# Kernel tuning notes

Measured on AMD Instinct MI355X. Metric: run time of the kernel, lower is better.

## Reference

```python
import jax, jax.numpy as jnp
import numpy as np

N = 20000
F_IN = 500
HID = 64
CLS = 16
H = 4
K_KNN = 10
NEG_SLOPE = 0.2


def _edges(key, n_rand):
    # random edges plus self-loops (mirrors add_self_loops in the torch code)
    src = jax.random.randint(key, (n_rand,), 0, N)
    dst = jax.random.randint(jax.random.fold_in(key, 1), (n_rand,), 0, N)
    loops = jnp.arange(N)
    return jnp.stack([jnp.concatenate([src, loops]), jnp.concatenate([dst, loops])]).astype(jnp.int32)


def setup_inputs():
    key = jax.random.key(0)
    ks = jax.random.split(key, 40)
    inp = {}
    inp['x'] = jax.random.normal(ks[0], (N, F_IN), jnp.float32)
    inp['edge_index_1'] = _edges(ks[1], 16 * N)          # 1-hop graph, 340k edges
    inp['edge_index_2'] = _edges(ks[2], 32 * N)          # denser 2-hop graph, 660k edges
    knn_src = jnp.repeat(jnp.arange(N), K_KNN)
    knn_dst = jax.random.randint(ks[3], (K_KNN * N,), 0, N)
    inp['edge_index_knn'] = jnp.stack([knn_src, knn_dst]).astype(jnp.int32)

    def p(k, shape):
        return jax.random.normal(k, shape, jnp.float32) * 0.05

    dims = {1: (F_IN, HID), 2: (HID, CLS), 3: (F_IN, HID), 4: (HID, CLS), 5: (F_IN, HID), 6: (HID, CLS)}
    i = 4
    for j in range(1, 7):
        fi, fo = dims[j]
        inp[f'W{j}'] = p(ks[i], (fi, H, fo)); i += 1
        inp[f'as{j}'] = p(ks[i], (H, fo)); i += 1
        inp[f'ad{j}'] = p(ks[i], (H, fo)); i += 1
        inp[f'b{j}'] = jnp.zeros((fo,), jnp.float32)
    for j in range(1, 4):
        inp[f'lin{j}_w'] = p(ks[i], (CLS, CLS)); i += 1
        inp[f'lin{j}_b'] = jnp.zeros((CLS,), jnp.float32)
    inp['agg_w'] = p(ks[i], (CLS,))
    return inp


def gat_conv(x, ei, W, a_s, a_d, b):
    # PyG GATConv, concat=False (mean over heads). W: [F,H,D], a_s/a_d: [H,D], b: [D]
    src, dst = ei[0], ei[1]
    z = jnp.einsum('nf,fhd->nhd', x, W)                 # [N,H,D]
    e_src = jnp.sum(z * a_s, -1)                         # [N,H]
    e_dst = jnp.sum(z * a_d, -1)                         # [N,H]
    e = jax.nn.leaky_relu(e_src[src] + e_dst[dst], NEG_SLOPE)   # [E,H]
    m = jax.ops.segment_max(e, dst, num_segments=N)      # per-dst softmax (edge softmax)
    p = jnp.exp(e - m[dst])
    s = jax.ops.segment_sum(p, dst, num_segments=N)
    alpha = p / (s[dst] + 1e-16)                         # [E,H]
    out = jax.ops.segment_sum(alpha[:, :, None] * z[src], dst, num_segments=N)  # [N,H,D]
    return out.mean(1) + b


def reference(x, edge_index_1, edge_index_2, edge_index_knn,
              W1, as1, ad1, b1, W2, as2, ad2, b2,
              W3, as3, ad3, b3, W4, as4, ad4, b4,
              W5, as5, ad5, b5, W6, as6, ad6, b6,
              lin1_w, lin1_b, lin2_w, lin2_b, lin3_w, lin3_b, agg_w):
    # eval mode: dropout is a no-op
    h1 = jax.nn.relu(gat_conv(x, edge_index_1, W1, as1, ad1, b1))
    h1 = gat_conv(h1, edge_index_1, W2, as2, ad2, b2)
    h2 = jax.nn.relu(gat_conv(x, edge_index_2, W3, as3, ad3, b3))
    h2 = gat_conv(h2, edge_index_2, W4, as4, ad4, b4)
    h3 = jax.nn.relu(gat_conv(x, edge_index_knn, W5, as5, ad5, b5))
    h3 = gat_conv(h3, edge_index_knn, W6, as6, ad6, b6)

    a1 = jnp.tanh(h1 @ lin1_w + lin1_b) @ agg_w          # [N]
    a2 = jnp.tanh(h2 @ lin2_w + lin2_b) @ agg_w
    a3 = jnp.tanh(h3 @ lin3_w + lin3_b) @ agg_w
    a = jax.nn.softmax(jnp.stack([a1, a2, a3], axis=1), axis=1)  # [N,3]
    h = a[:, 0:1] * h1 + a[:, 1:2] * h2 + a[:, 2:3] * h3
    return jax.nn.log_softmax(h, axis=1)
```

## Files before the change

kernel.cpp:

```cpp
#include <hip/hip_runtime.h>
#include <hip/hip_bf16.h>
#include <math.h>

#define N_NODES 20000
#define MP      20096
#define FIN     500
#define KP      512
#define NBUCK   157

typedef unsigned short u16;
typedef unsigned char  u8;
typedef __attribute__((ext_vector_type(8))) short   short8;
typedef __attribute__((ext_vector_type(2))) unsigned uv2;
typedef __attribute__((ext_vector_type(2))) float   f32x2;
typedef __attribute__((ext_vector_type(4))) float   f32x4;

__device__ __forceinline__ float b2f(u16 u){
  union { unsigned int i; float f; } v; v.i = ((unsigned int)u) << 16; return v.f;
}
__device__ __forceinline__ u16 f2b(float f){
  __hip_bfloat16 h = __float2bfloat16(f);
  return *reinterpret_cast<u16*>(&h);
}
__device__ __forceinline__ float lrelu(float x){ return x >= 0.f ? x : 0.2f * x; }
__device__ __forceinline__ float ldp(const void* p, int i, int bf){
  return bf ? b2f(((const u16*)p)[i]) : ((const float*)p)[i];
}
__device__ __forceinline__ u8 f2fp8(float f){
  return (u8)(__builtin_amdgcn_cvt_pk_fp8_f32(f, 0.f, 0, false) & 0xff);
}
template<bool HI>
__device__ __forceinline__ f32x2 fp8pair(unsigned w){
  return __builtin_amdgcn_cvt_pk_f32_fp8((int)w, HI);
}
__device__ __forceinline__ void gll16(const u16* g, u16* l){
  __builtin_amdgcn_global_load_lds(
      (const __attribute__((address_space(1))) unsigned int*)g,
      (__attribute__((address_space(3))) unsigned int*)l, 16, 0, 0);
}

__global__ void detect_dtype_kernel(const unsigned int* __restrict__ xw, int nwords,
                                    int* __restrict__ flag){
  __shared__ int cnt;
  if (threadIdx.x == 0) cnt = 0;
  __syncthreads();
  int c = 0;
  for (int i = threadIdx.x; i < nwords; i += 256){
    unsigned e = (xw[i] >> 7) & 0xFF;
    if (e >= 0x70 && e <= 0x8F) c++;
  }
  atomicAdd(&cnt, c);
  __syncthreads();
  if (threadIdx.x == 0) *flag = (cnt * 2 > nwords) ? 1 : 0;
}

#define CHA 8192
__global__ __launch_bounds__(256) void prep_kernel(
    const void* __restrict__ x, u16* __restrict__ xp,
    const void* Wb0, const void* Wb1, const void* Wb2,
    const void* Ws0, const void* Ws1, const void* Ws2,
    u16* ob0, u16* ob1, u16* ob2, u16* os0, u16* os1, u16* os2,
    const int* s0, const int* s1, const int* s2,
    const int* d0, const int* d1, const int* d2,
    int E0, int E1, int E2, int S0, int S1, int S2, int EB,
    int* __restrict__ bucketCur, unsigned* p0, unsigned* p1, unsigned* p2,
    const int* __restrict__ flag){
  __shared__ int hb[NBUCK];
  __shared__ int hbase[NBUCK];
  int bf = *flag;
  if (blockIdx.y == 0){
    int t = blockIdx.x * 256 + threadIdx.x;
    if (t >= MP * 64) return;
    int row = t >> 6;
    int j0  = (t & 63) * 8;
    short8 v;
#pragma unroll
    for (int j = 0; j < 8; ++j){
      int k = j0 + j;
      u16 val = 0;
      if (row < N_NODES && k < FIN)
        val = bf ? ((const u16*)x)[(size_t)row * FIN + k]
                 : f2b(((const float*)x)[(size_t)row * FIN + k]);
      v[j] = (short)val;
    }
    *(short8*)(xp + (size_t)row * KP + j0) = v;
  } else if (blockIdx.y == 1){
    int xb = blockIdx.x;
    if (xb >= 6 * 512) return;
    int which = xb >> 9;
    int t = (xb & 511) * 256 + threadIdx.x;
    if (which < 3){
      if (t >= 256 * KP) return;
      const void* W = which == 0 ? Wb0 : (which == 1 ? Wb1 : Wb2);
      u16* O = which == 0 ? ob0 : (which == 1 ? ob1 : ob2);
      int n = t / KP, k = t % KP;
      u16 val = 0;
      if (k < FIN)
        val = bf ? ((const u16*)W)[(size_t)k * 256 + n]
                 : f2b(((const float*)W)[(size_t)k * 256 + n]);
      O[t] = val;
    } else {
      if (t >= 64 * 64) return;
      const void* W = which == 3 ? Ws0 : (which == 4 ? Ws1 : Ws2);
      u16* O = which == 3 ? os0 : (which == 4 ? os1 : os2);
      int n = t / 64, k = t % 64;
      O[t] = bf ? ((const u16*)W)[(size_t)k * 64 + n]
                : f2b(((const float*)W)[(size_t)k * 64 + n]);
    }
  } else {
    int sblk = blockIdx.x;
    if (sblk >= 3 * EB) return;
    int g = sblk / EB;
    const int* src = g == 0 ? s0 : (g == 1 ? s1 : s2);
    const int* dst = g == 0 ? d0 : (g == 1 ? d1 : d2);
    unsigned* pairs = g == 0 ? p0 : (g == 1 ? p1 : p2);
    int E = g == 0 ? E0 : (g == 1 ? E1 : E2);
    int S = g == 0 ? S0 : (g == 1 ? S1 : S2);
    int base = (sblk % EB) * CHA;
    if (base >= E) return;
    for (int i = threadIdx.x; i < NBUCK; i += 256) hb[i] = 0;
    __syncthreads();
    int rk[CHA / 256];
#pragma unroll
    for (int i = 0; i < CHA / 256; ++i){
      int e = base + i * 256 + threadIdx.x;
      rk[i] = 0;
      if (e < E) rk[i] = atomicAdd(&hb[dst[e] >> 7], 1);
    }
    __syncthreads();
    for (int i = threadIdx.x; i < NBUCK; i += 256)
      hbase[i] = atomicAdd(&bucketCur[g * NBUCK + i], hb[i]);
    __syncthreads();
#pragma unroll
    for (int i = 0; i < CHA / 256; ++i){
      int e = base + i * 256 + threadIdx.x;
      if (e < E){
        int d = dst[e];
        int b = d >> 7;
        int pos = hbase[b] + rk[i];
        if (pos < S)
          pairs[(size_t)b * S + pos] = ((unsigned)src[e] << 7) | (unsigned)(d & 127);
      }
    }
  }
}

__global__ __launch_bounds__(256) void csr_finalize_kernel(
    const unsigned* p0, const unsigned* p1, const unsigned* p2,
    int S0, int S1, int S2,
    const int* __restrict__ bucketCur,
    int* e0, int* e1, int* e2,
    int2* __restrict__ metaB){
  int g = blockIdx.y;
  const unsigned* pairs = g == 0 ? p0 : (g == 1 ? p1 : p2);
  int* esrc = g == 0 ? e0 : (g == 1 ? e1 : e2);
  int S = g == 0 ? S0 : (g == 1 ? S1 : S2);
  int2* meta = metaB + (size_t)g * MP;
  int b = blockIdx.x;
  int nb = bucketCur[g * NBUCK + b];
  if (nb > S) nb = S;
  const unsigned* pb = pairs + (size_t)b * S;
  int* eb = esrc + (size_t)b * S;
  __shared__ int cnt[128];
  __shared__ int loff[128];
  __shared__ int cur[128];
  if (threadIdx.x < 128) cnt[threadIdx.x] = 0;
  __syncthreads();
  for (int i = threadIdx.x; i < nb; i += 256)
    atomicAdd(&cnt[pb[i] & 127], 1);
  __syncthreads();
  if (threadIdx.x == 0){
    int run = 0;
    for (int k = 0; k < 128; ++k){ loff[k] = run; run += cnt[k]; }
  }
  __syncthreads();
  if (threadIdx.x < 128){
    cur[threadIdx.x] = loff[threadIdx.x];
    int d = b * 128 + threadIdx.x;
    if (d < N_NODES){
      int2 m; m.x = b * S + loff[threadIdx.x]; m.y = cnt[threadIdx.x];
      meta[d] = m;
    }
  }
  __syncthreads();
  for (int i = threadIdx.x; i < nb; i += 256){
    unsigned u = pb[i];
    int slot = atomicAdd(&cur[u & 127], 1);
    eb[slot] = (int)(u >> 7);
  }
}

__global__ __launch_bounds__(256) void gemm_big_kernel(const u16* __restrict__ A,
    const u16* B0, const u16* B1, const u16* B2,
    u8* C0, u8* C1, u8* C2,
    const void* as0, const void* as1, const void* as2,
    const void* ad0, const void* ad1, const void* ad2,
    float* __restrict__ esB, float* __restrict__ edB,
    const int* __restrict__ flag, int M){
  int g = blockIdx.z;
  const u16* BT = g == 0 ? B0 : (g == 1 ? B1 : B2);
  u8* C = g == 0 ? C0 : (g == 1 ? C1 : C2);
  const void* as_ = g == 0 ? as0 : (g == 1 ? as1 : as2);
  const void* ad_ = g == 0 ? ad0 : (g == 1 ? ad1 : ad2);
  float* es = esB + (size_t)g * N_NODES * 4;
  float* ed = edB + (size_t)g * N_NODES * 4;
  __shared__ alignas(16) u16 As[128 * 64];
  __shared__ alignas(16) u16 Bs[128 * 64];
  const int K = KP, Nn = 256;
  int t = threadIdx.x, lane = t & 63, w = t >> 6;
  int m0 = blockIdx.y * 128, n0 = blockIdx.x * 128;
  int mw = (w >> 1) * 64, nw = (w & 1) * 64;
  f32x4 acc[4][4] = {};
  for (int k0 = 0; k0 < K; k0 += 64){
    __syncthreads();
#pragma unroll
    for (int i = 0; i < 4; ++i){
      int c = i * 256 + w * 64 + lane;
      int row = c >> 3, slot = c & 7;
      int kk = ((slot ^ (row & 7))) * 8;
      gll16(A  + (size_t)(m0 + row) * K + k0 + kk, As + (size_t)(i * 256 + w * 64) * 8);
      gll16(BT + (size_t)(n0 + row) * K + k0 + kk, Bs + (size_t)(i * 256 + w * 64) * 8);
    }
    __syncthreads();
#pragma unroll
    for (int ks = 0; ks < 2; ++ks){
      short8 af[4], bfr[4];
#pragma unroll
      for (int mi = 0; mi < 4; ++mi){
        int row = mw + mi * 16 + (lane & 15);
        int sl = (ks * 4 + (lane >> 4)) ^ (row & 7);
        af[mi] = *(const short8*)(As + (size_t)row * 64 + sl * 8);
      }
#pragma unroll
      for (int ni = 0; ni < 4; ++ni){
        int row = nw + ni * 16 + (lane & 15);
        int sl = (ks * 4 + (lane >> 4)) ^ (row & 7);
        bfr[ni] = *(const short8*)(Bs + (size_t)row * 64 + sl * 8);
      }
#pragma unroll
      for (int mi = 0; mi < 4; ++mi)
#pragma unroll
        for (int ni = 0; ni < 4; ++ni)
          acc[mi][ni] = __builtin_amdgcn_mfma_f32_16x16x32_bf16(af[mi], bfr[ni], acc[mi][ni], 0, 0, 0);
    }
  }
  int bf = *flag;
#pragma unroll
  for (int mi = 0; mi < 4; ++mi)
#pragma unroll
    for (int ni = 0; ni < 4; ++ni)
#pragma unroll
      for (int r = 0; r < 4; ++r){
        int row = m0 + mw + mi * 16 + (lane >> 4) * 4 + r;
        int col = n0 + nw + ni * 16 + (lane & 15);
        if (row < M) C[(size_t)row * Nn + col] = f2fp8(acc[mi][ni][r]);
      }
  {
    int h = (n0 + nw) >> 6;
    float asv[4], adv[4];
#pragma unroll
    for (int ni = 0; ni < 4; ++ni){
      int col = n0 + nw + ni * 16 + (lane & 15);
      asv[ni] = ldp(as_, col, bf);
      adv[ni] = ldp(ad_, col, bf);
    }
#pragma unroll
    for (int mi = 0; mi < 4; ++mi)
#pragma unroll
      for (int r = 0; r < 4; ++r){
        float ps = 0.f, pd2 = 0.f;
#pragma unroll
        for (int ni = 0; ni < 4; ++ni){
          ps  += acc[mi][ni][r] * asv[ni];
          pd2 += acc[mi][ni][r] * adv[ni];
        }
#pragma unroll
        for (int m2 = 1; m2 < 16; m2 <<= 1){
          ps  += __shfl_xor(ps, m2);
          pd2 += __shfl_xor(pd2, m2);
        }
        int row = m0 + mw + mi * 16 + (lane >> 4) * 4 + r;
        if ((lane & 15) == 0 && row < M){
          es[(size_t)row * 4 + h] = ps;
          ed[(size_t)row * 4 + h] = pd2;
        }
      }
  }
}

__global__ __launch_bounds__(256) void gemm_small_kernel(
    const u16* A0, const u16* A1, const u16* A2,
    const u16* B0, const u16* B1, const u16* B2,
    u8* C0, u8* C1, u8* C2,
    const void* as0, const void* as1, const void* as2,
    const void* ad0, const void* ad1, const void* ad2,
    float* __restrict__ esB, float* __restrict__ edB,
    const int* __restrict__ flag, int M){
  int g = blockIdx.y;
  const u16* A  = g == 0 ? A0 : (g == 1 ? A1 : A2);
  const u16* BT = g == 0 ? B0 : (g == 1 ? B1 : B2);
  u8* C = g == 0 ? C0 : (g == 1 ? C1 : C2);
  const void* as_ = g == 0 ? as0 : (g == 1 ? as1 : as2);
  const void* ad_ = g == 0 ? ad0 : (g == 1 ? ad1 : ad2);
  float* es = esB + (size_t)g * N_NODES * 4;
  float* ed = edB + (size_t)g * N_NODES * 4;
  __shared__ alignas(16) u16 As[64 * 64];
  __shared__ alignas(16) u16 Bs[64 * 64];
  int t = threadIdx.x, lane = t & 63, w = t >> 6;
  int m0 = blockIdx.x * 64;
#pragma unroll
  for (int i = 0; i < 2; ++i){
    int c = i * 256 + w * 64 + lane;
    int row = c >> 3, slot = c & 7;
    int kk = ((slot ^ (row & 7))) * 8;
    gll16(A  + (size_t)(m0 + row) * 64 + kk, As + (size_t)(i * 256 + w * 64) * 8);
    gll16(BT + (size_t)row * 64 + kk,        Bs + (size_t)(i * 256 + w * 64) * 8);
  }
  __syncthreads();
  f32x4 acc[4] = {};
  int mw = w * 16;
#pragma unroll
  for (int ks = 0; ks < 2; ++ks){
    int rowa = mw + (lane & 15);
    int sla = (ks * 4 + (lane >> 4)) ^ (rowa & 7);
    short8 af = *(const short8*)(As + (size_t)rowa * 64 + sla * 8);
#pragma unroll
    for (int ni = 0; ni < 4; ++ni){
      int rowb = ni * 16 + (lane & 15);
      int slb = (ks * 4 + (lane >> 4)) ^ (rowb & 7);
      short8 bv = *(const short8*)(Bs + (size_t)rowb * 64 + slb * 8);
      acc[ni] = __builtin_amdgcn_mfma_f32_16x16x32_bf16(af, bv, acc[ni], 0, 0, 0);
    }
  }
  int bf = *flag;
#pragma unroll
  for (int ni = 0; ni < 4; ++ni)
#pragma unroll
    for (int r = 0; r < 4; ++r){
      int row = m0 + mw + (lane >> 4) * 4 + r;
      int col = ni * 16 + (lane & 15);
      if (row < M) C[(size_t)row * 64 + col] = f2fp8(acc[ni][r]);
    }
  {
    float asv[4], adv[4];
#pragma unroll
    for (int ni = 0; ni < 4; ++ni){
      int col = ni * 16 + (lane & 15);
      asv[ni] = ldp(as_, col, bf);
      adv[ni] = ldp(ad_, col, bf);
    }
#pragma unroll
    for (int r = 0; r < 4; ++r){
      float ps[4], pd2[4];
#pragma unroll
      for (int ni = 0; ni < 4; ++ni){ ps[ni] = acc[ni][r] * asv[ni]; pd2[ni] = acc[ni][r] * adv[ni]; }
#pragma unroll
      for (int m2 = 1; m2 < 16; m2 <<= 1)
#pragma unroll
        for (int ni = 0; ni < 4; ++ni){
          ps[ni]  += __shfl_xor(ps[ni], m2);
          pd2[ni] += __shfl_xor(pd2[ni], m2);
        }
      int row = m0 + mw + (lane >> 4) * 4 + r;
      if ((lane & 15) == 0 && row < M){
#pragma unroll
        for (int ni = 0; ni < 4; ++ni){
          es[(size_t)row * 4 + ni] = ps[ni];
          ed[(size_t)row * 4 + ni] = pd2[ni];
        }
      }
    }
  }
}

template<int DT, bool RELU, bool BF16OUT, int PIPE>
__global__ __launch_bounds__(256) void gat_agg5_kernel(
    const u8* z0, const u8* z1, const u8* z2,
    const float* __restrict__ esB, const float* __restrict__ edB,
    const int2* __restrict__ metaB,
    const int* e0p, const int* e1p, const int* e2p,
    const void* b0, const void* b1, const void* b2,
    void* o0, void* o1, void* o2,
    const int* __restrict__ flag){
  int g = blockIdx.y;
  const u8* z = g == 0 ? z0 : (g == 1 ? z1 : z2);
  const int* esrc = g == 0 ? e0p : (g == 1 ? e1p : e2p);
  const void* bias = g == 0 ? b0 : (g == 1 ? b1 : b2);
  void* out = g == 0 ? o0 : (g == 1 ? o1 : o2);
  const float* es = esB + (size_t)g * N_NODES * 4;
  const float* ed = edB + (size_t)g * N_NODES * 4;
  const int2* meta = metaB + (size_t)g * MP;
  int bf = *flag;

  int d = (blockIdx.x * 256 + threadIdx.x) >> 6;
  int lane = threadIdx.x & 63;
  if (d >= N_NODES) return;
  constexpr int LPG = DT / 8;
  constexpr int G   = 64 / LPG;
  constexpr int HD  = DT / 4;
  int grp = lane / LPG;
  int li  = lane % LPG;
  int c0  = li * 8;
  int h   = c0 / HD;

  int2 md = meta[d];
  int deg = md.y;
  const int* ep = esrc + md.x;
  float edh = ed[(unsigned)d * 4 + h];

  float acc[8] = {0,0,0,0,0,0,0,0};
  float sacc = 0.f;

  int steps = (deg + PIPE * G - 1) / (PIPE * G);
  for (int tb = 0; tb < steps; ++tb){
    int e0 = tb * PIPE * G + grp;
    int s[PIPE]; float q[PIPE]; uv2 v[PIPE]; bool val[PIPE];
#pragma unroll
    for (int i = 0; i < PIPE; ++i){
      int e = e0 + i * G;
      val[i] = e < deg;
      int sl = ep[e];
      s[i] = val[i] ? sl : 0;
    }
#pragma unroll
    for (int i = 0; i < PIPE; ++i) q[i] = es[(unsigned)s[i] * 4 + h];
#pragma unroll
    for (int i = 0; i < PIPE; ++i) v[i] = *(const uv2*)(z + (unsigned)s[i] * DT + c0);
#pragma unroll
    for (int i = 0; i < PIPE; ++i){
      float p = val[i] ? __expf(lrelu(q[i] + edh)) : 0.f;
      sacc += p;
      f32x2 a0 = fp8pair<false>(v[i][0]), a1 = fp8pair<true>(v[i][0]);
      f32x2 a2 = fp8pair<false>(v[i][1]), a3 = fp8pair<true>(v[i][1]);
      acc[0] = fmaf(p, a0.x, acc[0]); acc[1] = fmaf(p, a0.y, acc[1]);
      acc[2] = fmaf(p, a1.x, acc[2]); acc[3] = fmaf(p, a1.y, acc[3]);
      acc[4] = fmaf(p, a2.x, acc[4]); acc[5] = fmaf(p, a2.y, acc[5]);
      acc[6] = fmaf(p, a3.x, acc[6]); acc[7] = fmaf(p, a3.y, acc[7]);
    }
  }

#pragma unroll
  for (int m = LPG; m < 64; m <<= 1){
    sacc += __shfl_xor(sacc, m);
#pragma unroll
    for (int j = 0; j < 8; ++j) acc[j] += __shfl_xor(acc[j], m);
  }
  float inv = 1.f / (sacc + 1e-16f);
  float v8[8];
#pragma unroll
  for (int j = 0; j < 8; ++j) v8[j] = acc[j] * inv;
#pragma unroll
  for (int m = HD / 8; m < LPG; m <<= 1)
#pragma unroll
    for (int j = 0; j < 8; ++j) v8[j] += __shfl_xor(v8[j], m);

  if (lane < HD / 8){
    if constexpr (BF16OUT){
      short8 ov;
#pragma unroll
      for (int j = 0; j < 8; ++j){
        float o = v8[j] * 0.25f + ldp(bias, lane * 8 + j, bf);
        if (RELU) o = fmaxf(o, 0.f);
        ov[j] = (short)f2b(o);
      }
      *(short8*)((u16*)out + (size_t)d * HD + lane * 8) = ov;
    } else {
      float o[8];
#pragma unroll
      for (int j = 0; j < 8; ++j){
        o[j] = v8[j] * 0.25f + ldp(bias, lane * 8 + j, bf);
        if (RELU) o[j] = fmaxf(o[j], 0.f);
      }
      float* op = (float*)out + (size_t)d * HD + lane * 8;
      *(float4*)op = make_float4(o[0], o[1], o[2], o[3]);
      *(float4*)(op + 4) = make_float4(o[4], o[5], o[6], o[7]);
    }
  }
}

__global__ __launch_bounds__(256) void final_combine_kernel(
    const float* __restrict__ h1, const float* __restrict__ h2, const float* __restrict__ h3,
    const void* l1w, const void* l1b, const void* l2w, const void* l2b,
    const void* l3w, const void* l3b, const void* aggw,
    void* __restrict__ outv, int n, const int* __restrict__ flag){
  __shared__ float Lw[3][16][16];
  __shared__ float Lb[3][16];
  __shared__ float Ag[16];
  int t = threadIdx.x;
  int bf = *flag;
  {
    const void* ws[3] = { l1w, l2w, l3w };
    for (int g = 0; g < 3; ++g) Lw[g][t / 16][t % 16] = ldp(ws[g], t, bf);
    if (t < 16){
      Lb[0][t] = ldp(l1b, t, bf); Lb[1][t] = ldp(l2b, t, bf); Lb[2][t] = ldp(l3b, t, bf);
      Ag[t] = ldp(aggw, t, bf);
    }
  }
  __syncthreads();
  int node = blockIdx.x * 256 + t;
  if (node >= n) return;
  const float* hp[3] = { h1, h2, h3 };
  float hv[3][16];
  float a[3];
  for (int g = 0; g < 3; ++g){
    const float4* h4 = (const float4*)(hp[g] + (size_t)node * 16);
#pragma unroll
    for (int q = 0; q < 4; ++q){
      float4 f = h4[q];
      hv[g][q * 4 + 0] = f.x; hv[g][q * 4 + 1] = f.y;
      hv[g][q * 4 + 2] = f.z; hv[g][q * 4 + 3] = f.w;
    }
    float dot = 0.f;
#pragma unroll
    for (int j = 0; j < 16; ++j){
      float acc2 = Lb[g][j];
#pragma unroll
      for (int i = 0; i < 16; ++i) acc2 += hv[g][i] * Lw[g][i][j];
      dot += tanhf(acc2) * Ag[j];
    }
    a[g] = dot;
  }
  float am = fmaxf(a[0], fmaxf(a[1], a[2]));
  float e0 = __expf(a[0] - am), e1 = __expf(a[1] - am), e2 = __expf(a[2] - am);
  float einv = 1.f / (e0 + e1 + e2);
  float w0 = e0 * einv, w1 = e1 * einv, w2 = e2 * einv;
  float hh[16];
  float hmax = -INFINITY;
#pragma unroll
  for (int i = 0; i < 16; ++i){
    hh[i] = w0 * hv[0][i] + w1 * hv[1][i] + w2 * hv[2][i];
    hmax = fmaxf(hmax, hh[i]);
  }
  float se = 0.f;
#pragma unroll
  for (int i = 0; i < 16; ++i) se += __expf(hh[i] - hmax);
  float ls = hmax + logf(se);
#pragma unroll
  for (int i = 0; i < 16; ++i){
    float o = hh[i] - ls;
    if (bf) ((__hip_bfloat16*)outv)[(size_t)node * 16 + i] = __float2bfloat16(o);
    else    ((float*)outv)[(size_t)node * 16 + i] = o;
  }
}

extern "C" void kernel_launch(void* const* d_in, const int* in_sizes, int n_in,
                              void* d_out, int out_size, void* d_ws, size_t ws_size,
                              hipStream_t stream){
  const void* x = d_in[0];
  const int* ei[3] = { (const int*)d_in[1], (const int*)d_in[2], (const int*)d_in[3] };
  int E[3] = { in_sizes[1] / 2, in_sizes[2] / 2, in_sizes[3] / 2 };
  int Emax = E[0] > E[1] ? E[0] : E[1]; if (E[2] > Emax) Emax = E[2];
  int EB = (Emax + CHA - 1) / CHA;
  int S[3];
  for (int g = 0; g < 3; ++g){
    long s = ((long)E[g] * 27 / 20) / NBUCK + 64;
    s &= ~63L; if (s > 8192) s = 8192;
    S[g] = (int)s;
  }
  const void *W[6], *as_[6], *ad_[6], *bb[6];
  for (int j = 0; j < 6; ++j){
    W[j]   = d_in[4 + 4 * j];
    as_[j] = d_in[5 + 4 * j];
    ad_[j] = d_in[6 + 4 * j];
    bb[j]  = d_in[7 + 4 * j];
  }
  const void* l1w = d_in[28]; const void* l1b = d_in[29];
  const void* l2w = d_in[30]; const void* l2b = d_in[31];
  const void* l3w = d_in[32]; const void* l3b = d_in[33];
  const void* agg = d_in[34];

  char* p = (char*)d_ws;
  auto alloc = [&](size_t bytes) -> void* {
    void* r = (void*)p;
    p += (bytes + 255) & ~(size_t)255;
    return r;
  };
  int* dflag = (int*)alloc(256);
  u16* xp = (u16*)alloc((size_t)MP * KP * 2);
  u16* hmid[3]; for (int g = 0; g < 3; ++g) hmid[g] = xp + (size_t)g * MP * 64;
  u16* wtb[3]; for (int g = 0; g < 3; ++g) wtb[g] = (u16*)alloc((size_t)256 * KP * 2);
  u16* wts[3]; for (int g = 0; g < 3; ++g) wts[g] = (u16*)alloc((size_t)64 * 64 * 2);
  u8* zf[3];   for (int g = 0; g < 3; ++g) zf[g]  = (u8*)alloc((size_t)N_NODES * 256 + 256);
  float* hbr[3]; for (int g = 0; g < 3; ++g) hbr[g] = (float*)alloc((size_t)N_NODES * 16 * 4);
  float* esB = (float*)alloc((size_t)3 * N_NODES * 4 * 4);
  float* edB = (float*)alloc((size_t)3 * N_NODES * 4 * 4);
  int* bucketCur = (int*)alloc((size_t)3 * NBUCK * 4);
  int2* metaB    = (int2*)alloc((size_t)3 * MP * 8);
  int* esrc[3];
  for (int g = 0; g < 3; ++g) esrc[g] = (int*)alloc(((size_t)NBUCK * S[g] + 256) * 4);
  unsigned* pairs[3];
  for (int g = 0; g < 3; ++g) pairs[g] = (unsigned*)alloc(((size_t)NBUCK * S[g] + 256) * 4);

  const int* s0 = ei[0];          const int* s1 = ei[1];          const int* s2 = ei[2];
  const int* d0 = ei[0] + E[0];   const int* d1 = ei[1] + E[1];   const int* d2 = ei[2] + E[2];

  (void)hipMemsetAsync(bucketCur, 0, (size_t)3 * NBUCK * 4, stream);
  detect_dtype_kernel<<<1, 256, 0, stream>>>((const unsigned int*)x, 16384, dflag);
  prep_kernel<<<dim3((MP * 64 + 255) / 256, 3), 256, 0, stream>>>(
      x, xp, W[0], W[2], W[4], W[1], W[3], W[5],
      wtb[0], wtb[1], wtb[2], wts[0], wts[1], wts[2],
      s0, s1, s2, d0, d1, d2, E[0], E[1], E[2], S[0], S[1], S[2], EB,
      bucketCur, pairs[0], pairs[1], pairs[2], dflag);
  csr_finalize_kernel<<<dim3(NBUCK, 3), 256, 0, stream>>>(
      pairs[0], pairs[1], pairs[2], S[0], S[1], S[2], bucketCur,
      esrc[0], esrc[1], esrc[2], metaB);

  const int convGrid = (N_NODES + 3) / 4;

  gemm_big_kernel<<<dim3(2, MP / 128, 3), 256, 0, stream>>>(
      xp, wtb[0], wtb[1], wtb[2], zf[0], zf[1], zf[2],
      as_[0], as_[2], as_[4], ad_[0], ad_[2], ad_[4], esB, edB, dflag, N_NODES);
  gat_agg5_kernel<256, true, true, 6><<<dim3(convGrid, 3), 256, 0, stream>>>(
      zf[0], zf[1], zf[2], esB, edB, metaB, esrc[0], esrc[1], esrc[2],
      bb[0], bb[2], bb[4], (void*)hmid[0], (void*)hmid[1], (void*)hmid[2], dflag);

  gemm_small_kernel<<<dim3(MP / 64, 3), 256, 0, stream>>>(
      hmid[0], hmid[1], hmid[2], wts[0], wts[1], wts[2], zf[0], zf[1], zf[2],
      as_[1], as_[3], as_[5], ad_[1], ad_[3], ad_[5], esB, edB, dflag, N_NODES);
  gat_agg5_kernel<64, false, false, 4><<<dim3(convGrid, 3), 256, 0, stream>>>(
      zf[0], zf[1], zf[2], esB, edB, metaB, esrc[0], esrc[1], esrc[2],
      bb[1], bb[3], bb[5], (void*)hbr[0], (void*)hbr[1], (void*)hbr[2], dflag);

  final_combine_kernel<<<(N_NODES + 255) / 256, 256, 0, stream>>>(
      hbr[0], hbr[1], hbr[2], l1w, l1b, l2w, l2b, l3w, l3b, agg,
      d_out, N_NODES, dflag);
}
```

Before: 366.5 us.

## Rework prep kernel: vectorized x cast, tiled weight transpose, LDS-staged edge bucketing

Prep and CSR kernels move to 1024-thread blocks. The x conversion now uses vectorized float4/ushort4 loads. Weight transposes go through a 64x65 LDS tile so both reads and writes are coalesced. Edge bucketing sorts each chunk locally in LDS before scattering, so global writes to the pairs buffer are contiguous per bucket. The dtype detection also samples fewer words. In exchange the prep kernel uses much more LDS, and every branch of it pays that allocation.

```diff
diff --git a/kernel.cpp b/kernel.cpp
--- a/kernel.cpp
+++ b/kernel.cpp
@@ -38,14 +38,19 @@
       (const __attribute__((address_space(1))) unsigned int*)g,
       (__attribute__((address_space(3))) unsigned int*)l, 16, 0, 0);
 }
-
-__global__ void detect_dtype_kernel(const unsigned int* __restrict__ xw, int nwords,
-                                    int* __restrict__ flag){
+__device__ __forceinline__ void barrier_lgkm(){
+  asm volatile("s_waitcnt lgkmcnt(0)" ::: "memory");
+  __builtin_amdgcn_s_barrier();
+  asm volatile("" ::: "memory");
+}
+
+__global__ __launch_bounds__(1024) void detect_dtype_kernel(const unsigned int* __restrict__ xw, int nwords,
+                                                            int* __restrict__ flag){
   __shared__ int cnt;
   if (threadIdx.x == 0) cnt = 0;
   __syncthreads();
   int c = 0;
-  for (int i = threadIdx.x; i < nwords; i += 256){
+  for (int i = threadIdx.x; i < nwords; i += 1024){
     unsigned e = (xw[i] >> 7) & 0xFF;
     if (e >= 0x70 && e <= 0x8F) c++;
   }
@@ -55,7 +60,8 @@
 }
 
 #define CHA 8192
-__global__ __launch_bounds__(256) void prep_kernel(
+#define PB  1024
+__global__ __launch_bounds__(PB) void prep_kernel(
     const void* __restrict__ x, u16* __restrict__ xp,
     const void* Wb0, const void* Wb1, const void* Wb2,
     const void* Ws0, const void* Ws1, const void* Ws2,
@@ -66,46 +72,78 @@
     int* __restrict__ bucketCur, unsigned* p0, unsigned* p1, unsigned* p2,
     const int* __restrict__ flag){
   __shared__ int hb[NBUCK];
+  __shared__ int loff[NBUCK];
   __shared__ int hbase[NBUCK];
+  __shared__ unsigned shp[CHA];
+  __shared__ u8 shb[CHA];
+  __shared__ u16 tile[64][65];
   int bf = *flag;
+  int tid = threadIdx.x;
   if (blockIdx.y == 0){
-    int t = blockIdx.x * 256 + threadIdx.x;
+    int t = blockIdx.x * PB + tid;
     if (t >= MP * 64) return;
     int row = t >> 6;
     int j0  = (t & 63) * 8;
-    short8 v;
-#pragma unroll
-    for (int j = 0; j < 8; ++j){
-      int k = j0 + j;
-      u16 val = 0;
-      if (row < N_NODES && k < FIN)
-        val = bf ? ((const u16*)x)[(size_t)row * FIN + k]
-                 : f2b(((const float*)x)[(size_t)row * FIN + k]);
-      v[j] = (short)val;
+    short8 v = {0,0,0,0,0,0,0,0};
+    if (row < N_NODES){
+      if (j0 + 8 <= FIN){
+        if (bf){
+          const ushort4* xr = (const ushort4*)((const u16*)x + (size_t)row * FIN + j0);
+          ushort4 a = xr[0], b = xr[1];
+          v[0]=(short)a.x; v[1]=(short)a.y; v[2]=(short)a.z; v[3]=(short)a.w;
+          v[4]=(short)b.x; v[5]=(short)b.y; v[6]=(short)b.z; v[7]=(short)b.w;
+        } else {
+          const float4* xr = (const float4*)((const float*)x + (size_t)row * FIN + j0);
+          float4 a = xr[0], b = xr[1];
+          v[0]=(short)f2b(a.x); v[1]=(short)f2b(a.y); v[2]=(short)f2b(a.z); v[3]=(short)f2b(a.w);
+          v[4]=(short)f2b(b.x); v[5]=(short)f2b(b.y); v[6]=(short)f2b(b.z); v[7]=(short)f2b(b.w);
+        }
+      } else {
+#pragma unroll
+        for (int j = 0; j < 8; ++j){
+          int k = j0 + j;
+          u16 val = 0;
+          if (k < FIN)
+            val = bf ? ((const u16*)x)[(size_t)row * FIN + k]
+                     : f2b(((const float*)x)[(size_t)row * FIN + k]);
+          v[j] = (short)val;
+        }
+      }
     }
     *(short8*)(xp + (size_t)row * KP + j0) = v;
   } else if (blockIdx.y == 1){
     int xb = blockIdx.x;
-    if (xb >= 6 * 512) return;
-    int which = xb >> 9;
-    int t = (xb & 511) * 256 + threadIdx.x;
-    if (which < 3){
-      if (t >= 256 * KP) return;
-      const void* W = which == 0 ? Wb0 : (which == 1 ? Wb1 : Wb2);
-      u16* O = which == 0 ? ob0 : (which == 1 ? ob1 : ob2);
-      int n = t / KP, k = t % KP;
-      u16 val = 0;
-      if (k < FIN)
-        val = bf ? ((const u16*)W)[(size_t)k * 256 + n]
-                 : f2b(((const float*)W)[(size_t)k * 256 + n]);
-      O[t] = val;
+    if (xb >= 96 + 3) return;
+    int tx = tid & 63, tyb = tid >> 6;
+    const void* Wsrc; u16* O; int SRCW, SRCH, DSTW, kt, nt;
+    if (xb < 96){
+      int which = xb >> 5, tl = xb & 31;
+      nt = (tl & 3) << 6; kt = (tl >> 2) << 6;
+      Wsrc = which == 0 ? Wb0 : (which == 1 ? Wb1 : Wb2);
+      O    = which == 0 ? ob0 : (which == 1 ? ob1 : ob2);
+      SRCW = 256; SRCH = FIN; DSTW = KP;
     } else {
-      if (t >= 64 * 64) return;
-      const void* W = which == 3 ? Ws0 : (which == 4 ? Ws1 : Ws2);
-      u16* O = which == 3 ? os0 : (which == 4 ? os1 : os2);
-      int n = t / 64, k = t % 64;
-      O[t] = bf ? ((const u16*)W)[(size_t)k * 64 + n]
-                : f2b(((const float*)W)[(size_t)k * 64 + n]);
+      int which = xb - 96;
+      nt = 0; kt = 0;
+      Wsrc = which == 0 ? Ws0 : (which == 1 ? Ws1 : Ws2);
+      O    = which == 0 ? os0 : (which == 1 ? os1 : os2);
+      SRCW = 64; SRCH = 64; DSTW = 64;
+    }
+#pragma unroll
+    for (int r = 0; r < 4; ++r){
+      int kl = tyb + r * 16;
+      int k = kt + kl, n = nt + tx;
+      u16 vv = 0;
+      if (k < SRCH)
+        vv = bf ? ((const u16*)Wsrc)[(size_t)k * SRCW + n]
+                : f2b(((const float*)Wsrc)[(size_t)k * SRCW + n]);
+      tile[kl][tx] = vv;
+    }
+    __syncthreads();
+#pragma unroll
+    for (int r = 0; r < 4; ++r){
+      int nl = tyb + r * 16;
+      O[(size_t)(nt + nl) * DSTW + kt + tx] = tile[tx][nl];
     }
   } else {
     int sblk = blockIdx.x;
@@ -118,34 +156,50 @@
     int S = g == 0 ? S0 : (g == 1 ? S1 : S2);
     int base = (sblk % EB) * CHA;
     if (base >= E) return;
-    for (int i = threadIdx.x; i < NBUCK; i += 256) hb[i] = 0;
+    if (tid < NBUCK) hb[tid] = 0;
     __syncthreads();
-    int rk[CHA / 256];
-#pragma unroll
-    for (int i = 0; i < CHA / 256; ++i){
-      int e = base + i * 256 + threadIdx.x;
-      rk[i] = 0;
-      if (e < E) rk[i] = atomicAdd(&hb[dst[e] >> 7], 1);
+    constexpr int EPT = CHA / PB;
+    int rk[EPT]; unsigned pr[EPT]; int bk[EPT]; bool vl[EPT];
+#pragma unroll
+    for (int i = 0; i < EPT; ++i){
+      int e = base + i * PB + tid;
+      vl[i] = e < E;
+      bk[i] = 0; rk[i] = 0; pr[i] = 0;
+      if (vl[i]){
+        int dd = dst[e], ss = src[e];
+        bk[i] = dd >> 7;
+        pr[i] = ((unsigned)ss << 7) | (unsigned)(dd & 127);
+        rk[i] = atomicAdd(&hb[bk[i]], 1);
+      }
     }
     __syncthreads();
-    for (int i = threadIdx.x; i < NBUCK; i += 256)
-      hbase[i] = atomicAdd(&bucketCur[g * NBUCK + i], hb[i]);
+    int ret = 0;
+    if (tid < NBUCK) ret = atomicAdd(&bucketCur[g * NBUCK + tid], hb[tid]);
+    if (tid == 0){
+      int run = 0;
+      for (int k = 0; k < NBUCK; ++k){ loff[k] = run; run += hb[k]; }
+    }
+    barrier_lgkm();
+#pragma unroll
+    for (int i = 0; i < EPT; ++i)
+      if (vl[i]){
+        int j = loff[bk[i]] + rk[i];
+        shp[j] = pr[i];
+        shb[j] = (u8)bk[i];
+      }
+    if (tid < NBUCK) hbase[tid] = ret;
     __syncthreads();
-#pragma unroll
-    for (int i = 0; i < CHA / 256; ++i){
-      int e = base + i * 256 + threadIdx.x;
-      if (e < E){
-        int d = dst[e];
-        int b = d >> 7;
-        int pos = hbase[b] + rk[i];
-        if (pos < S)
-          pairs[(size_t)b * S + pos] = ((unsigned)src[e] << 7) | (unsigned)(d & 127);
-      }
-    }
-  }
-}
-
-__global__ __launch_bounds__(256) void csr_finalize_kernel(
+    int nb = E - base; if (nb > CHA) nb = CHA;
+    for (int j = tid; j < nb; j += PB){
+      int b = shb[j];
+      int pos = hbase[b] + (j - loff[b]);
+      if (pos < S)
+        pairs[(size_t)b * S + pos] = shp[j];
+    }
+  }
+}
+
+__global__ __launch_bounds__(1024) void csr_finalize_kernel(
     const unsigned* p0, const unsigned* p1, const unsigned* p2,
     int S0, int S1, int S2,
     const int* __restrict__ bucketCur,
@@ -166,7 +220,7 @@
   __shared__ int cur[128];
   if (threadIdx.x < 128) cnt[threadIdx.x] = 0;
   __syncthreads();
-  for (int i = threadIdx.x; i < nb; i += 256)
+  for (int i = threadIdx.x; i < nb; i += 1024)
     atomicAdd(&cnt[pb[i] & 127], 1);
   __syncthreads();
   if (threadIdx.x == 0){
@@ -183,7 +237,7 @@
     }
   }
   __syncthreads();
-  for (int i = threadIdx.x; i < nb; i += 256){
+  for (int i = threadIdx.x; i < nb; i += 1024){
     unsigned u = pb[i];
     int slot = atomicAdd(&cur[u & 127], 1);
     eb[slot] = (int)(u >> 7);
@@ -595,13 +649,13 @@
   const int* d0 = ei[0] + E[0];   const int* d1 = ei[1] + E[1];   const int* d2 = ei[2] + E[2];
 
   (void)hipMemsetAsync(bucketCur, 0, (size_t)3 * NBUCK * 4, stream);
-  detect_dtype_kernel<<<1, 256, 0, stream>>>((const unsigned int*)x, 16384, dflag);
-  prep_kernel<<<dim3((MP * 64 + 255) / 256, 3), 256, 0, stream>>>(
+  detect_dtype_kernel<<<1, 1024, 0, stream>>>((const unsigned int*)x, 4096, dflag);
+  prep_kernel<<<dim3((MP * 64 + PB - 1) / PB, 3), PB, 0, stream>>>(
       x, xp, W[0], W[2], W[4], W[1], W[3], W[5],
       wtb[0], wtb[1], wtb[2], wts[0], wts[1], wts[2],
       s0, s1, s2, d0, d1, d2, E[0], E[1], E[2], S[0], S[1], S[2], EB,
       bucketCur, pairs[0], pairs[1], pairs[2], dflag);
-  csr_finalize_kernel<<<dim3(NBUCK, 3), 256, 0, stream>>>(
+  csr_finalize_kernel<<<dim3(NBUCK, 3), 1024, 0, stream>>>(
       pairs[0], pairs[1], pairs[2], S[0], S[1], S[2], bucketCur,
       esrc[0], esrc[1], esrc[2], metaB);
 
```

Measured after the change: 331.2 us. -9.6%, faster.
